# Kernel optimization log

Measured on AMD Instinct MI355X. Metric: run time of the kernel, lower is better.

## Reference

```python
import jax, jax.numpy as jnp
import numpy as np

INPUT_DIM = 128
HIDDEN_DIM = 128
WINDOW_SIZE = 256
BLOCK_SIZE = 256
BATCH = 8
SEQ = 8192


def setup_inputs() -> dict:
    key = jax.random.key(0)
    ks = jax.random.split(key, 7)
    s = 1.0 / np.sqrt(INPUT_DIM)
    return {
        "x": jax.random.normal(ks[0], (BATCH, SEQ, INPUT_DIM), dtype=jnp.float32),
        "Wq": jax.random.normal(ks[1], (HIDDEN_DIM, INPUT_DIM), dtype=jnp.float32) * s,
        "bq": jax.random.normal(ks[2], (HIDDEN_DIM,), dtype=jnp.float32) * s,
        "Wk": jax.random.normal(ks[3], (HIDDEN_DIM, INPUT_DIM), dtype=jnp.float32) * s,
        "bk": jax.random.normal(ks[4], (HIDDEN_DIM,), dtype=jnp.float32) * s,
        "Wv": jax.random.normal(ks[5], (HIDDEN_DIM, INPUT_DIM), dtype=jnp.float32) * s,
        "bv": jax.random.normal(ks[6], (HIDDEN_DIM,), dtype=jnp.float32) * s,
    }


def reference(x, Wq, bq, Wk, bk, Wv, bv):
    B, S, D = x.shape
    bs, w = BLOCK_SIZE, WINDOW_SIZE
    nb = S // bs
    halo = w - 1
    W = bs + 2 * halo  # per-block K/V window width

    q = x @ Wq.T + bq  # [B,S,H]
    k = x @ Wk.T + bk
    v = x @ Wv.T + bv

    # Zero-pad K/V by halo on both sides. Since there is NO softmax, padded
    # zero keys give zero scores and padded zero values contribute zero —
    # this exactly reproduces the torch code's clamped window slicing.
    k_pad = jnp.pad(k, ((0, 0), (halo, halo), (0, 0)))
    v_pad = jnp.pad(v, ((0, 0), (halo, halo), (0, 0)))

    # Gather overlapping windows: [B, nb, W, H]
    starts = jnp.arange(nb) * bs  # window start in padded coords
    idx = starts[:, None] + jnp.arange(W)[None, :]  # [nb, W]
    k_win = k_pad[:, idx, :]
    v_win = v_pad[:, idx, :]

    q_blk = q.reshape(B, nb, bs, -1)  # [B, nb, bs, H]

    scale = 1.0 / jnp.sqrt(jnp.float32(D))
    attn = jnp.einsum('bnqh,bnkh->bnqk', q_blk, k_win) * scale  # no softmax
    out = jnp.einsum('bnqk,bnkh->bnqh', attn, v_win)
    return out.reshape(B, S, -1)
```

## Files before the change

kernel.cpp:

```cpp
#include <hip/hip_runtime.h>
#include <stdint.h>


#define B_ 8
#define S_ 8192

using bf16x8 = __attribute__((ext_vector_type(8))) short;
using s16x4  = __attribute__((ext_vector_type(4))) short;
using f32x16 = __attribute__((ext_vector_type(16))) float;

__device__ __forceinline__ short f2bf(float f) {
  union { float f; uint32_t u; } v; v.f = f;
  uint32_t r = v.u + 0x7fffu + ((v.u >> 16) & 1u);
  return (short)(r >> 16);
}

#define LDW 136

__global__ __launch_bounds__(256) void proj_kernel(
    const float* __restrict__ x,
    const float* __restrict__ Wq, const float* __restrict__ bq,
    const float* __restrict__ Wk, const float* __restrict__ bk,
    const float* __restrict__ Wv, const float* __restrict__ bv,
    short* __restrict__ qb, short* __restrict__ ktb, short* __restrict__ vtb)
{
  __shared__ short wl[128 * LDW];

  const int tid  = threadIdx.x;
  const int lane = tid & 63;
  const int wv   = tid >> 6;
  const int c    = lane & 31;
  const int hl   = lane >> 5;
  const int r0   = blockIdx.x * 128;
  const int b    = r0 >> 13;
  const int s0   = r0 & (S_ - 1);

  bf16x8 afrag[8];
  {
    const float* xrow = x + (size_t)(r0 + wv * 32 + c) * 128 + hl * 8;
    #pragma unroll
    for (int kst = 0; kst < 8; ++kst) {
      const float4* p = (const float4*)(xrow + kst * 16);
      float4 f0 = p[0], f1 = p[1];
      bf16x8 a;
      a[0] = f2bf(f0.x); a[1] = f2bf(f0.y); a[2] = f2bf(f0.z); a[3] = f2bf(f0.w);
      a[4] = f2bf(f1.x); a[5] = f2bf(f1.y); a[6] = f2bf(f1.z); a[7] = f2bf(f1.w);
      afrag[kst] = a;
    }
  }

  auto stageW = [&](const float* W) {
    #pragma unroll
    for (int it = 0; it < 16; ++it) {
      int l  = it * 256 + tid;
      int n  = l >> 5;
      int k4 = (l & 31) << 2;
      const float4 f = *(const float4*)(W + n * 128 + k4);
      s16x4 o;
      o[0] = f2bf(f.x); o[1] = f2bf(f.y); o[2] = f2bf(f.z); o[3] = f2bf(f.w);
      *(s16x4*)(wl + n * LDW + k4) = o;
    }
  };

  auto gemm = [&](const float* bias, f32x16* acc) {
    #pragma unroll
    for (int nt = 0; nt < 4; ++nt) {
      float bvv = bias[nt * 32 + c];
      #pragma unroll
      for (int i = 0; i < 16; ++i) acc[nt][i] = bvv;
    }
    #pragma unroll
    for (int kst = 0; kst < 8; ++kst) {
      #pragma unroll
      for (int nt = 0; nt < 4; ++nt) {
        bf16x8 bb = *(const bf16x8*)(wl + (nt * 32 + c) * LDW + kst * 16 + hl * 8);
        acc[nt] = __builtin_amdgcn_mfma_f32_32x32x16_bf16(afrag[kst], bb, acc[nt], 0, 0, 0);
      }
    }
  };

  auto writeTransposedLDS = [&](f32x16* acc) {
    #pragma unroll
    for (int nt = 0; nt < 4; ++nt) {
      int d = nt * 32 + c;
      #pragma unroll
      for (int g = 0; g < 4; ++g) {
        #pragma unroll
        for (int p = 0; p < 2; ++p) {
          int reg = g * 4 + p * 2;
          int sl  = wv * 32 + g * 8 + hl * 4 + p * 2;
          uint32_t pk = (uint32_t)(uint16_t)f2bf(acc[nt][reg]) |
                        ((uint32_t)(uint16_t)f2bf(acc[nt][reg + 1]) << 16);
          *(uint32_t*)(wl + d * LDW + sl) = pk;
        }
      }
    }
  };

  auto storeTransposed = [&](short* dst) {
    #pragma unroll
    for (int it = 0; it < 8; ++it) {
      int l  = it * 256 + tid;
      int d  = l >> 4;
      int s8 = (l & 15) << 3;
      bf16x8 vv = *(const bf16x8*)(wl + d * LDW + s8);
      *(bf16x8*)(dst + ((size_t)b * 128 + d) * S_ + s0 + s8) = vv;
    }
  };

  stageW(Wq);
  __syncthreads();
  {
    f32x16 acc[4];
    gemm(bq, acc);
    __syncthreads();
    #pragma unroll
    for (int nt = 0; nt < 4; ++nt) {
      #pragma unroll
      for (int reg = 0; reg < 16; ++reg) {
        int row = (reg & 3) + 8 * (reg >> 2) + 4 * hl;
        wl[(wv * 32 + row) * LDW + nt * 32 + c] = f2bf(acc[nt][reg]);
      }
    }
    __syncthreads();
    #pragma unroll
    for (int it = 0; it < 8; ++it) {
      int l  = it * 256 + tid;
      int s  = l >> 4;
      int d8 = (l & 15) << 3;
      bf16x8 vv = *(const bf16x8*)(wl + s * LDW + d8);
      *(bf16x8*)(qb + (size_t)(r0 + s) * 128 + d8) = vv;
    }
  }
  __syncthreads();

  stageW(Wk);
  __syncthreads();
  {
    f32x16 acc[4];
    gemm(bk, acc);
    __syncthreads();
    writeTransposedLDS(acc);
    __syncthreads();
    storeTransposed(ktb);
  }
  __syncthreads();

  stageW(Wv);
  __syncthreads();
  {
    f32x16 acc[4];
    gemm(bv, acc);
    __syncthreads();
    writeTransposedLDS(acc);
    __syncthreads();
    storeTransposed(vtb);
  }
}

#define LDC 72
#define LDM 136
#define BUFB 36864

__global__ __launch_bounds__(512) void attn_kernel(
    const short* __restrict__ qb, const short* __restrict__ ktb,
    const short* __restrict__ vtb, float* __restrict__ out)
{
  __shared__ __align__(16) char smem[2 * BUFB + BUFB];
  short* m_l  = (short*)smem;
  float* opat = (float*)(smem + 2 * BUFB);

  const int tid  = threadIdx.x;
  const int lane = tid & 63;
  const int wv   = tid >> 6;
  const int c    = lane & 31;
  const int hl   = lane >> 5;
  const int b    = blockIdx.x >> 5;
  const int n    = blockIdx.x & 31;

  const int win_lo = (n == 0) ? 0 : n * 256 - 255;
  const int win_hi = (n == 31) ? S_ : n * 256 + 511;
  const int jlo = (n == 0) ? 4 : 0;
  const int jhi = (n == 31) ? 8 : 12;
  const int cbase = n * 256 - 256;

  const short* ktb_b = ktb + (size_t)b * 128 * S_;
  const short* vtb_b = vtb + (size_t)b * 128 * S_;

  const int ht = wv >> 1;
  const int dh = wv & 1;

  const int sd  = tid >> 3;
  const int ss8 = (tid & 7) << 3;

  f32x16 macc[2];
  #pragma unroll
  for (int ntl = 0; ntl < 2; ++ntl)
    #pragma unroll
    for (int i = 0; i < 16; ++i) macc[ntl][i] = 0.f;

  auto loadChunk = [&](int c0, bf16x8* pk, bf16x8* pv) {
    #pragma unroll
    for (int it = 0; it < 2; ++it) {
      int d  = sd + it * 64;
      int sb = c0 + ss8;
      pk[it] = *(const bf16x8*)(ktb_b + (size_t)d * S_ + sb);
      pv[it] = *(const bf16x8*)(vtb_b + (size_t)d * S_ + sb);
    }
  };

  auto storeChunk = [&](int c0, short* buf, bf16x8* pk, bf16x8* pv) {
    short* ktc = buf;
    short* vtc = buf + 128 * LDC;
    int sb = c0 + ss8;
    bool edge = (sb < win_lo) || (sb + 7 >= win_hi);
    #pragma unroll
    for (int it = 0; it < 2; ++it) {
      bf16x8 kv = pk[it];
      if (edge) {
        #pragma unroll
        for (int e = 0; e < 8; ++e)
          if (sb + e < win_lo || sb + e >= win_hi) kv[e] = 0;
      }
      int d = sd + it * 64;
      *(bf16x8*)(ktc + d * LDC + ss8) = kv;
      *(bf16x8*)(vtc + d * LDC + ss8) = pv[it];
    }
  };

  auto mfmaChunk = [&](short* buf) {
    short* ktc = buf;
    short* vtc = buf + 128 * LDC;
    #pragma unroll
    for (int kst = 0; kst < 4; ++kst) {
      bf16x8 a = *(const bf16x8*)(vtc + (ht * 32 + c) * LDC + kst * 16 + hl * 8);
      #pragma unroll
      for (int ntl = 0; ntl < 2; ++ntl) {
        int nt = dh * 2 + ntl;
        bf16x8 bb = *(const bf16x8*)(ktc + (nt * 32 + c) * LDC + kst * 16 + hl * 8);
        macc[ntl] = __builtin_amdgcn_mfma_f32_32x32x16_bf16(a, bb, macc[ntl], 0, 0, 0);
      }
    }
  };

  {
    bf16x8 pk[2], pv[2];
    loadChunk(cbase + jlo * 64, pk, pv);
    storeChunk(cbase + jlo * 64, (short*)smem, pk, pv);
  }
  __syncthreads();

  for (int j = jlo; j < jhi; ++j) {
    short* cur = (short*)(smem + (size_t)(((j - jlo) & 1) ? BUFB : 0));
    short* nxt = (short*)(smem + (size_t)(((j - jlo) & 1) ? 0 : BUFB));
    bf16x8 pk[2], pv[2];
    const bool more = (j + 1 < jhi);
    if (more) loadChunk(cbase + (j + 1) * 64, pk, pv);
    mfmaChunk(cur);
    if (more) storeChunk(cbase + (j + 1) * 64, nxt, pk, pv);
    __syncthreads();
  }

  bf16x8 qf[8];
  {
    const short* q0p = qb + ((size_t)b * S_ + n * 256 + wv * 32 + c) * 128 + hl * 8;
    #pragma unroll
    for (int kst = 0; kst < 8; ++kst) qf[kst] = *(const bf16x8*)(q0p + kst * 16);
  }

  const float scale = 0.08838834764831845f;
  #pragma unroll
  for (int ntl = 0; ntl < 2; ++ntl) {
    #pragma unroll
    for (int reg = 0; reg < 16; ++reg) {
      int row = (reg & 3) + 8 * (reg >> 2) + 4 * hl;
      m_l[(ht * 32 + row) * LDM + (dh * 2 + ntl) * 32 + c] =
          f2bf(macc[ntl][reg] * scale);
    }
  }
  __syncthreads();

  f32x16 oacc[4];
  #pragma unroll
  for (int nt = 0; nt < 4; ++nt)
    #pragma unroll
    for (int i = 0; i < 16; ++i) oacc[nt][i] = 0.f;

  #pragma unroll
  for (int kst = 0; kst < 8; ++kst) {
    #pragma unroll
    for (int nt = 0; nt < 4; ++nt) {
      bf16x8 bb = *(const bf16x8*)(m_l + (nt * 32 + c) * LDM + kst * 16 + hl * 8);
      oacc[nt] = __builtin_amdgcn_mfma_f32_32x32x16_bf16(qf[kst], bb, oacc[nt], 0, 0, 0);
    }
  }

  float* patch = opat + wv * (32 * 36);
  float* outb  = out + ((size_t)b * S_ + n * 256 + wv * 32) * 128;
  #pragma unroll
  for (int nt = 0; nt < 4; ++nt) {
    #pragma unroll
    for (int reg = 0; reg < 16; ++reg) {
      int row = (reg & 3) + 8 * (reg >> 2) + 4 * hl;
      patch[row * 36 + c] = oacc[nt][reg];
    }
    #pragma unroll
    for (int p = 0; p < 4; ++p) {
      int row = p * 8 + (lane >> 3);
      float4 vv = *(const float4*)(patch + row * 36 + (lane & 7) * 4);
      *(float4*)(outb + (size_t)row * 128 + nt * 32 + (lane & 7) * 4) = vv;
    }
  }
}

extern "C" void kernel_launch(void* const* d_in, const int* in_sizes, int n_in,
                              void* d_out, int out_size, void* d_ws, size_t ws_size,
                              hipStream_t stream) {
  const float* x  = (const float*)d_in[0];
  const float* Wq = (const float*)d_in[1];
  const float* bq = (const float*)d_in[2];
  const float* Wk = (const float*)d_in[3];
  const float* bk = (const float*)d_in[4];
  const float* Wv = (const float*)d_in[5];
  const float* bv = (const float*)d_in[6];
  float* out = (float*)d_out;

  const size_t elems = (size_t)B_ * S_ * 128;
  short* qb  = (short*)d_ws;
  short* ktb = qb + elems;
  short* vtb = ktb + elems;

  proj_kernel<<<512, 256, 0, stream>>>(x, Wq, bq, Wk, bk, Wv, bv, qb, ktb, vtb);
  attn_kernel<<<256, 512, 0, stream>>>(qb, ktb, vtb, out);
}
```

Baseline: 123.6 us.

## Fuse QKV projection into windowed attention kernel, recomputing K/V per window

Merges the projection and attention kernels into one launch, so each block projects its own K/V chunks from x straight into LDS and projects Q locally. This removes the bf16 Q/K/V workspace round trip through global memory and the second launch. In exchange, K/V projection is recomputed for the overlapping windows (about 3x redundant projection work) and more x is read per block. Block indices are also swizzled so blocks that run together touch different batches.

Result: slower. 224.4 us (+81.6%).

```diff
diff --git a/kernel.cpp b/kernel.cpp
--- a/kernel.cpp
+++ b/kernel.cpp
@@ -4,9 +4,12 @@
 
 #define B_ 8
 #define S_ 8192
+#define LDC 72
+#define LDM 136
+#define LDQ 136
+#define BUFB 36864
 
 using bf16x8 = __attribute__((ext_vector_type(8))) short;
-using s16x4  = __attribute__((ext_vector_type(4))) short;
 using f32x16 = __attribute__((ext_vector_type(16))) float;
 
 __device__ __forceinline__ short f2bf(float f) {
@@ -15,277 +18,253 @@
   return (short)(r >> 16);
 }
 
-#define LDW 136
-
-__global__ __launch_bounds__(256) void proj_kernel(
+__device__ __forceinline__ bf16x8 cvt8(float4 a, float4 b) {
+  bf16x8 r;
+  r[0] = f2bf(a.x); r[1] = f2bf(a.y); r[2] = f2bf(a.z); r[3] = f2bf(a.w);
+  r[4] = f2bf(b.x); r[5] = f2bf(b.y); r[6] = f2bf(b.z); r[7] = f2bf(b.w);
+  return r;
+}
+
+__global__ __launch_bounds__(512) void fused_kernel(
     const float* __restrict__ x,
     const float* __restrict__ Wq, const float* __restrict__ bq,
     const float* __restrict__ Wk, const float* __restrict__ bk,
     const float* __restrict__ Wv, const float* __restrict__ bv,
-    short* __restrict__ qb, short* __restrict__ ktb, short* __restrict__ vtb)
+    float* __restrict__ out)
 {
-  __shared__ short wl[128 * LDW];
+  __shared__ __align__(16) char smem[106496];
 
   const int tid  = threadIdx.x;
   const int lane = tid & 63;
   const int wv   = tid >> 6;
   const int c    = lane & 31;
   const int hl   = lane >> 5;
-  const int r0   = blockIdx.x * 128;
-  const int b    = r0 >> 13;
-  const int s0   = r0 & (S_ - 1);
-
-  bf16x8 afrag[8];
+
+  const int swz = (blockIdx.x & 7) * 32 + (blockIdx.x >> 3);
+  const int b   = swz >> 5;
+  const int n   = swz & 31;
+
+  const int win_lo = (n == 0) ? 0 : n * 256 - 255;
+  const int win_hi = (n == 31) ? S_ : n * 256 + 511;
+  const int jlo    = (n == 0) ? 4 : 0;
+  const int jhi    = (n == 31) ? 8 : 12;
+  const int cbase  = n * 256 - 256;
+
+  const float* xb = x + (size_t)b * S_ * 128;
+
+  const bool is_k = (wv < 4);
+  const int  pw   = wv & 3;
+  const int  rt   = pw & 1;
+  const int  ctp  = pw >> 1;
+  const float* Wrole = is_k ? Wk : Wv;
+  const float* brole = is_k ? bk : bv;
+
+  bf16x8 wfrag[2][8];
+  float  bias2[2];
+  #pragma unroll
+  for (int t = 0; t < 2; ++t) {
+    const int ct = 2 * ctp + t;
+    bias2[t] = brole[ct * 32 + c];
+    const float* wr = Wrole + (size_t)(ct * 32 + c) * 128 + hl * 8;
+    #pragma unroll
+    for (int kst = 0; kst < 8; ++kst) {
+      float4 f0 = *(const float4*)(wr + kst * 16);
+      float4 f1 = *(const float4*)(wr + kst * 16 + 4);
+      wfrag[t][kst] = cvt8(f0, f1);
+    }
+  }
+
+  f32x16 macc[2];
+  #pragma unroll
+  for (int t = 0; t < 2; ++t)
+    #pragma unroll
+    for (int i = 0; i < 16; ++i) macc[t][i] = 0.f;
+
+  bf16x8 af[8];
   {
-    const float* xrow = x + (size_t)(r0 + wv * 32 + c) * 128 + hl * 8;
+    const float* xr = xb + (size_t)(cbase + jlo * 64 + rt * 32 + c) * 128 + hl * 8;
     #pragma unroll
     for (int kst = 0; kst < 8; ++kst) {
-      const float4* p = (const float4*)(xrow + kst * 16);
-      float4 f0 = p[0], f1 = p[1];
-      bf16x8 a;
-      a[0] = f2bf(f0.x); a[1] = f2bf(f0.y); a[2] = f2bf(f0.z); a[3] = f2bf(f0.w);
-      a[4] = f2bf(f1.x); a[5] = f2bf(f1.y); a[6] = f2bf(f1.z); a[7] = f2bf(f1.w);
-      afrag[kst] = a;
-    }
-  }
-
-  auto stageW = [&](const float* W) {
-    #pragma unroll
-    for (int it = 0; it < 16; ++it) {
-      int l  = it * 256 + tid;
-      int n  = l >> 5;
-      int k4 = (l & 31) << 2;
-      const float4 f = *(const float4*)(W + n * 128 + k4);
-      s16x4 o;
-      o[0] = f2bf(f.x); o[1] = f2bf(f.y); o[2] = f2bf(f.z); o[3] = f2bf(f.w);
-      *(s16x4*)(wl + n * LDW + k4) = o;
-    }
-  };
-
-  auto gemm = [&](const float* bias, f32x16* acc) {
-    #pragma unroll
-    for (int nt = 0; nt < 4; ++nt) {
-      float bvv = bias[nt * 32 + c];
-      #pragma unroll
-      for (int i = 0; i < 16; ++i) acc[nt][i] = bvv;
-    }
-    #pragma unroll
-    for (int kst = 0; kst < 8; ++kst) {
-      #pragma unroll
-      for (int nt = 0; nt < 4; ++nt) {
-        bf16x8 bb = *(const bf16x8*)(wl + (nt * 32 + c) * LDW + kst * 16 + hl * 8);
-        acc[nt] = __builtin_amdgcn_mfma_f32_32x32x16_bf16(afrag[kst], bb, acc[nt], 0, 0, 0);
-      }
-    }
-  };
-
-  auto writeTransposedLDS = [&](f32x16* acc) {
-    #pragma unroll
-    for (int nt = 0; nt < 4; ++nt) {
-      int d = nt * 32 + c;
+      float4 f0 = *(const float4*)(xr + kst * 16);
+      float4 f1 = *(const float4*)(xr + kst * 16 + 4);
+      af[kst] = cvt8(f0, f1);
+    }
+  }
+
+  for (int j = jlo; j < jhi; ++j) {
+    const int jj = j - jlo;
+    short* ktc = (short*)(smem + (size_t)(jj & 1) * BUFB);
+    short* vtc = ktc + 128 * LDC;
+    const int c0 = cbase + j * 64;
+    const bool more = (j + 1 < jhi);
+
+    float4 fx[16];
+    if (more) {
+      const float* xr = xb + (size_t)(c0 + 64 + rt * 32 + c) * 128 + hl * 8;
+      #pragma unroll
+      for (int kst = 0; kst < 8; ++kst) {
+        fx[2 * kst]     = *(const float4*)(xr + kst * 16);
+        fx[2 * kst + 1] = *(const float4*)(xr + kst * 16 + 4);
+      }
+    }
+
+    f32x16 cacc[2];
+    #pragma unroll
+    for (int t = 0; t < 2; ++t)
+      #pragma unroll
+      for (int i = 0; i < 16; ++i) cacc[t][i] = bias2[t];
+    #pragma unroll
+    for (int kst = 0; kst < 8; ++kst)
+      #pragma unroll
+      for (int t = 0; t < 2; ++t)
+        cacc[t] = __builtin_amdgcn_mfma_f32_32x32x16_bf16(af[kst], wfrag[t][kst], cacc[t], 0, 0, 0);
+
+    short* dst = is_k ? ktc : vtc;
+    const bool maskme = is_k && ((c0 < win_lo) | (c0 + 64 > win_hi));
+    #pragma unroll
+    for (int t = 0; t < 2; ++t) {
+      const int d = (2 * ctp + t) * 32 + c;
       #pragma unroll
       for (int g = 0; g < 4; ++g) {
         #pragma unroll
         for (int p = 0; p < 2; ++p) {
-          int reg = g * 4 + p * 2;
-          int sl  = wv * 32 + g * 8 + hl * 4 + p * 2;
-          uint32_t pk = (uint32_t)(uint16_t)f2bf(acc[nt][reg]) |
-                        ((uint32_t)(uint16_t)f2bf(acc[nt][reg + 1]) << 16);
-          *(uint32_t*)(wl + d * LDW + sl) = pk;
+          const int reg = g * 4 + p * 2;
+          const int sl  = rt * 32 + g * 8 + hl * 4 + p * 2;
+          float v0 = cacc[t][reg], v1 = cacc[t][reg + 1];
+          if (maskme) {
+            const int sg = c0 + sl;
+            if (sg < win_lo || sg >= win_hi) v0 = 0.f;
+            if (sg + 1 < win_lo || sg + 1 >= win_hi) v1 = 0.f;
+          }
+          const uint32_t pk = (uint32_t)(uint16_t)f2bf(v0) |
+                              ((uint32_t)(uint16_t)f2bf(v1) << 16);
+          *(uint32_t*)(dst + d * LDC + sl) = pk;
         }
       }
     }
-  };
-
-  auto storeTransposed = [&](short* dst) {
-    #pragma unroll
-    for (int it = 0; it < 8; ++it) {
-      int l  = it * 256 + tid;
-      int d  = l >> 4;
-      int s8 = (l & 15) << 3;
-      bf16x8 vv = *(const bf16x8*)(wl + d * LDW + s8);
-      *(bf16x8*)(dst + ((size_t)b * 128 + d) * S_ + s0 + s8) = vv;
-    }
-  };
-
-  stageW(Wq);
+    __syncthreads();
+
+    {
+      const int ht = wv >> 1, dh = wv & 1;
+      #pragma unroll
+      for (int kst = 0; kst < 4; ++kst) {
+        bf16x8 a = *(const bf16x8*)(vtc + (ht * 32 + c) * LDC + kst * 16 + hl * 8);
+        #pragma unroll
+        for (int ntl = 0; ntl < 2; ++ntl) {
+          bf16x8 bb = *(const bf16x8*)(ktc + ((dh * 2 + ntl) * 32 + c) * LDC + kst * 16 + hl * 8);
+          macc[ntl] = __builtin_amdgcn_mfma_f32_32x32x16_bf16(a, bb, macc[ntl], 0, 0, 0);
+        }
+      }
+    }
+
+    if (more) {
+      #pragma unroll
+      for (int kst = 0; kst < 8; ++kst)
+        af[kst] = cvt8(fx[2 * kst], fx[2 * kst + 1]);
+    }
+  }
+
+  short* m_l = (short*)smem;
+  short* q_l = (short*)(smem + BUFB);
+
+  const int rt2 = wv & 3;
+  const int qcp = wv >> 2;
+  const int qs0 = n * 256;
+
+  float4 fxq[32];
+  #pragma unroll
+  for (int t = 0; t < 2; ++t) {
+    const float* xr = xb + (size_t)(qs0 + rt2 * 64 + t * 32 + c) * 128 + hl * 8;
+    #pragma unroll
+    for (int kst = 0; kst < 8; ++kst) {
+      fxq[t * 16 + 2 * kst]     = *(const float4*)(xr + kst * 16);
+      fxq[t * 16 + 2 * kst + 1] = *(const float4*)(xr + kst * 16 + 4);
+    }
+  }
+
+  const float scale = 0.08838834764831845f;
+  {
+    const int ht = wv >> 1, dh = wv & 1;
+    #pragma unroll
+    for (int ntl = 0; ntl < 2; ++ntl) {
+      #pragma unroll
+      for (int reg = 0; reg < 16; ++reg) {
+        const int row = (reg & 3) + 8 * (reg >> 2) + 4 * hl;
+        m_l[(ht * 32 + row) * LDM + (dh * 2 + ntl) * 32 + c] =
+            f2bf(macc[ntl][reg] * scale);
+      }
+    }
+  }
+
+  bf16x8 aq[2][8];
+  #pragma unroll
+  for (int t = 0; t < 2; ++t)
+    #pragma unroll
+    for (int kst = 0; kst < 8; ++kst)
+      aq[t][kst] = cvt8(fxq[t * 16 + 2 * kst], fxq[t * 16 + 2 * kst + 1]);
+
+  float4 fwq[32];
+  float  qbias[2];
+  #pragma unroll
+  for (int t = 0; t < 2; ++t) {
+    const int ct = 2 * qcp + t;
+    qbias[t] = bq[ct * 32 + c];
+    const float* wr = Wq + (size_t)(ct * 32 + c) * 128 + hl * 8;
+    #pragma unroll
+    for (int kst = 0; kst < 8; ++kst) {
+      fwq[t * 16 + 2 * kst]     = *(const float4*)(wr + kst * 16);
+      fwq[t * 16 + 2 * kst + 1] = *(const float4*)(wr + kst * 16 + 4);
+    }
+  }
+
   __syncthreads();
-  {
-    f32x16 acc[4];
-    gemm(bq, acc);
-    __syncthreads();
-    #pragma unroll
-    for (int nt = 0; nt < 4; ++nt) {
+
+  bf16x8 wq[2][8];
+  #pragma unroll
+  for (int t = 0; t < 2; ++t)
+    #pragma unroll
+    for (int kst = 0; kst < 8; ++kst)
+      wq[t][kst] = cvt8(fwq[t * 16 + 2 * kst], fwq[t * 16 + 2 * kst + 1]);
+
+  f32x16 qacc[2][2];
+  #pragma unroll
+  for (int a = 0; a < 2; ++a)
+    #pragma unroll
+    for (int t = 0; t < 2; ++t)
+      #pragma unroll
+      for (int i = 0; i < 16; ++i) qacc[a][t][i] = qbias[t];
+  #pragma unroll
+  for (int kst = 0; kst < 8; ++kst)
+    #pragma unroll
+    for (int a = 0; a < 2; ++a)
+      #pragma unroll
+      for (int t = 0; t < 2; ++t)
+        qacc[a][t] = __builtin_amdgcn_mfma_f32_32x32x16_bf16(aq[a][kst], wq[t][kst], qacc[a][t], 0, 0, 0);
+
+  #pragma unroll
+  for (int a = 0; a < 2; ++a) {
+    #pragma unroll
+    for (int t = 0; t < 2; ++t) {
       #pragma unroll
       for (int reg = 0; reg < 16; ++reg) {
-        int row = (reg & 3) + 8 * (reg >> 2) + 4 * hl;
-        wl[(wv * 32 + row) * LDW + nt * 32 + c] = f2bf(acc[nt][reg]);
-      }
-    }
-    __syncthreads();
-    #pragma unroll
-    for (int it = 0; it < 8; ++it) {
-      int l  = it * 256 + tid;
-      int s  = l >> 4;
-      int d8 = (l & 15) << 3;
-      bf16x8 vv = *(const bf16x8*)(wl + s * LDW + d8);
-      *(bf16x8*)(qb + (size_t)(r0 + s) * 128 + d8) = vv;
+        const int row = rt2 * 64 + a * 32 + (reg & 3) + 8 * (reg >> 2) + 4 * hl;
+        q_l[row * LDQ + (2 * qcp + t) * 32 + c] = f2bf(qacc[a][t][reg]);
+      }
     }
   }
   __syncthreads();
-
-  stageW(Wk);
-  __syncthreads();
-  {
-    f32x16 acc[4];
-    gemm(bk, acc);
-    __syncthreads();
-    writeTransposedLDS(acc);
-    __syncthreads();
-    storeTransposed(ktb);
-  }
-  __syncthreads();
-
-  stageW(Wv);
-  __syncthreads();
-  {
-    f32x16 acc[4];
-    gemm(bv, acc);
-    __syncthreads();
-    writeTransposedLDS(acc);
-    __syncthreads();
-    storeTransposed(vtb);
-  }
-}
-
-#define LDC 72
-#define LDM 136
-#define BUFB 36864
-
-__global__ __launch_bounds__(512) void attn_kernel(
-    const short* __restrict__ qb, const short* __restrict__ ktb,
-    const short* __restrict__ vtb, float* __restrict__ out)
-{
-  __shared__ __align__(16) char smem[2 * BUFB + BUFB];
-  short* m_l  = (short*)smem;
-  float* opat = (float*)(smem + 2 * BUFB);
-
-  const int tid  = threadIdx.x;
-  const int lane = tid & 63;
-  const int wv   = tid >> 6;
-  const int c    = lane & 31;
-  const int hl   = lane >> 5;
-  const int b    = blockIdx.x >> 5;
-  const int n    = blockIdx.x & 31;
-
-  const int win_lo = (n == 0) ? 0 : n * 256 - 255;
-  const int win_hi = (n == 31) ? S_ : n * 256 + 511;
-  const int jlo = (n == 0) ? 4 : 0;
-  const int jhi = (n == 31) ? 8 : 12;
-  const int cbase = n * 256 - 256;
-
-  const short* ktb_b = ktb + (size_t)b * 128 * S_;
-  const short* vtb_b = vtb + (size_t)b * 128 * S_;
-
-  const int ht = wv >> 1;
-  const int dh = wv & 1;
-
-  const int sd  = tid >> 3;
-  const int ss8 = (tid & 7) << 3;
-
-  f32x16 macc[2];
-  #pragma unroll
-  for (int ntl = 0; ntl < 2; ++ntl)
-    #pragma unroll
-    for (int i = 0; i < 16; ++i) macc[ntl][i] = 0.f;
-
-  auto loadChunk = [&](int c0, bf16x8* pk, bf16x8* pv) {
-    #pragma unroll
-    for (int it = 0; it < 2; ++it) {
-      int d  = sd + it * 64;
-      int sb = c0 + ss8;
-      pk[it] = *(const bf16x8*)(ktb_b + (size_t)d * S_ + sb);
-      pv[it] = *(const bf16x8*)(vtb_b + (size_t)d * S_ + sb);
-    }
-  };
-
-  auto storeChunk = [&](int c0, short* buf, bf16x8* pk, bf16x8* pv) {
-    short* ktc = buf;
-    short* vtc = buf + 128 * LDC;
-    int sb = c0 + ss8;
-    bool edge = (sb < win_lo) || (sb + 7 >= win_hi);
-    #pragma unroll
-    for (int it = 0; it < 2; ++it) {
-      bf16x8 kv = pk[it];
-      if (edge) {
-        #pragma unroll
-        for (int e = 0; e < 8; ++e)
-          if (sb + e < win_lo || sb + e >= win_hi) kv[e] = 0;
-      }
-      int d = sd + it * 64;
-      *(bf16x8*)(ktc + d * LDC + ss8) = kv;
-      *(bf16x8*)(vtc + d * LDC + ss8) = pv[it];
-    }
-  };
-
-  auto mfmaChunk = [&](short* buf) {
-    short* ktc = buf;
-    short* vtc = buf + 128 * LDC;
-    #pragma unroll
-    for (int kst = 0; kst < 4; ++kst) {
-      bf16x8 a = *(const bf16x8*)(vtc + (ht * 32 + c) * LDC + kst * 16 + hl * 8);
-      #pragma unroll
-      for (int ntl = 0; ntl < 2; ++ntl) {
-        int nt = dh * 2 + ntl;
-        bf16x8 bb = *(const bf16x8*)(ktc + (nt * 32 + c) * LDC + kst * 16 + hl * 8);
-        macc[ntl] = __builtin_amdgcn_mfma_f32_32x32x16_bf16(a, bb, macc[ntl], 0, 0, 0);
-      }
-    }
-  };
-
-  {
-    bf16x8 pk[2], pv[2];
-    loadChunk(cbase + jlo * 64, pk, pv);
-    storeChunk(cbase + jlo * 64, (short*)smem, pk, pv);
-  }
-  __syncthreads();
-
-  for (int j = jlo; j < jhi; ++j) {
-    short* cur = (short*)(smem + (size_t)(((j - jlo) & 1) ? BUFB : 0));
-    short* nxt = (short*)(smem + (size_t)(((j - jlo) & 1) ? 0 : BUFB));
-    bf16x8 pk[2], pv[2];
-    const bool more = (j + 1 < jhi);
-    if (more) loadChunk(cbase + (j + 1) * 64, pk, pv);
-    mfmaChunk(cur);
-    if (more) storeChunk(cbase + (j + 1) * 64, nxt, pk, pv);
-    __syncthreads();
-  }
 
   bf16x8 qf[8];
   {
-    const short* q0p = qb + ((size_t)b * S_ + n * 256 + wv * 32 + c) * 128 + hl * 8;
-    #pragma unroll
-    for (int kst = 0; kst < 8; ++kst) qf[kst] = *(const bf16x8*)(q0p + kst * 16);
-  }
-
-  const float scale = 0.08838834764831845f;
-  #pragma unroll
-  for (int ntl = 0; ntl < 2; ++ntl) {
-    #pragma unroll
-    for (int reg = 0; reg < 16; ++reg) {
-      int row = (reg & 3) + 8 * (reg >> 2) + 4 * hl;
-      m_l[(ht * 32 + row) * LDM + (dh * 2 + ntl) * 32 + c] =
-          f2bf(macc[ntl][reg] * scale);
-    }
-  }
-  __syncthreads();
-
+    const short* qrow = q_l + (wv * 32 + c) * LDQ + hl * 8;
+    #pragma unroll
+    for (int kst = 0; kst < 8; ++kst) qf[kst] = *(const bf16x8*)(qrow + kst * 16);
+  }
   f32x16 oacc[4];
   #pragma unroll
   for (int nt = 0; nt < 4; ++nt)
     #pragma unroll
     for (int i = 0; i < 16; ++i) oacc[nt][i] = 0.f;
-
   #pragma unroll
   for (int kst = 0; kst < 8; ++kst) {
     #pragma unroll
@@ -294,19 +273,20 @@
       oacc[nt] = __builtin_amdgcn_mfma_f32_32x32x16_bf16(qf[kst], bb, oacc[nt], 0, 0, 0);
     }
   }
-
-  float* patch = opat + wv * (32 * 36);
+  __syncthreads();
+
+  float* patch = (float*)(smem + BUFB) + wv * (32 * 36);
   float* outb  = out + ((size_t)b * S_ + n * 256 + wv * 32) * 128;
   #pragma unroll
   for (int nt = 0; nt < 4; ++nt) {
     #pragma unroll
     for (int reg = 0; reg < 16; ++reg) {
-      int row = (reg & 3) + 8 * (reg >> 2) + 4 * hl;
+      const int row = (reg & 3) + 8 * (reg >> 2) + 4 * hl;
       patch[row * 36 + c] = oacc[nt][reg];
     }
     #pragma unroll
     for (int p = 0; p < 4; ++p) {
-      int row = p * 8 + (lane >> 3);
+      const int row = p * 8 + (lane >> 3);
       float4 vv = *(const float4*)(patch + row * 36 + (lane & 7) * 4);
       *(float4*)(outb + (size_t)row * 128 + nt * 32 + (lane & 7) * 4) = vv;
     }
@@ -325,11 +305,5 @@
   const float* bv = (const float*)d_in[6];
   float* out = (float*)d_out;
 
-  const size_t elems = (size_t)B_ * S_ * 128;
-  short* qb  = (short*)d_ws;
-  short* ktb = qb + elems;
-  short* vtb = ktb + elems;
-
-  proj_kernel<<<512, 256, 0, stream>>>(x, Wq, bq, Wk, bk, Wv, bv, qb, ktb, vtb);
-  attn_kernel<<<256, 512, 0, stream>>>(qb, ktb, vtb, out);
+  fused_kernel<<<256, 512, 0, stream>>>(x, Wq, bq, Wk, bk, Wv, bv, out);
 }
```
